# Kernel tuning notes

Measured on AMD Instinct MI355X. Metric: run time of the kernel, lower is better.

Reference implementation:

```python
import jax, jax.numpy as jnp
import numpy as np

TOPK = 8

def setup_inputs() -> dict:
    key = jax.random.key(0)
    k1, k2, k3, k4 = jax.random.split(key, 4)
    B, T, D = 4, 4096, 1024
    SUB, HALF, VDIM = 512, D // 2, 128
    query = jax.random.normal(k1, (B, T, D), dtype=jnp.float32)
    codebook1 = jax.random.normal(k2, (SUB, HALF), dtype=jnp.float32) * 0.02
    codebook2 = jax.random.normal(k3, (SUB, HALF), dtype=jnp.float32) * 0.02
    values = jax.random.normal(k4, (SUB * SUB, VDIM), dtype=jnp.float32) * 0.02
    return {"query": query, "codebook1": codebook1, "codebook2": codebook2, "values": values}

def reference(query, codebook1, codebook2, values):
    B, T, D = query.shape
    sub_keys, half = codebook1.shape
    q1 = query[..., :half]
    q2 = query[..., half:2 * half]
    # [B,T,sub_keys] score matrices
    s1 = jnp.einsum('btd,kd->btk', q1, codebook1)
    s2 = jnp.einsum('btd,kd->btk', q2, codebook2)
    tk1_vals, tk1_idx = jax.lax.top_k(s1, TOPK)
    tk2_vals, tk2_idx = jax.lax.top_k(s2, TOPK)
    # cartesian combine: [B,T,TOPK,TOPK] -> [B,T,TOPK*TOPK]
    full_idx = (tk1_idx[..., :, None] * sub_keys + tk2_idx[..., None, :]).reshape(B, T, -1)
    w1 = jax.nn.softmax(tk1_vals, axis=-1)
    w2 = jax.nn.softmax(tk2_vals, axis=-1)
    weights = (w1[..., :, None] * w2[..., None, :]).reshape(B, T, -1)
    vals = values[full_idx]  # [B,T,TOPK^2,value_dim] gather
    return jnp.einsum('btk,btkv->btv', weights, vals)
```

## Files before the change

kernel.cpp:

```cpp
#include <hip/hip_runtime.h>
#include <hip/hip_bf16.h>
#include <math.h>

#define NTOK 16384
#define DDIM 1024
#define HALF 512
#define SUB  512
#define KDIM 512
#define TOPK 8
#define NCAND 16
#define VDIM 128
#define TMB 16

typedef __attribute__((ext_vector_type(8))) short bf16x8;
typedef __attribute__((ext_vector_type(4))) float f32x4;

static __device__ __forceinline__ unsigned short f2bf(float x) {
    union { float f; unsigned u; } v; v.f = x;
    unsigned r = v.u + 0x7FFF + ((v.u >> 16) & 1);
    return (unsigned short)(r >> 16);
}

static __device__ __forceinline__ void split_bf(float x, unsigned short& h, unsigned short& l) {
    h = f2bf(x);
    union { unsigned u; float f; } hv; hv.u = ((unsigned)h) << 16;
    l = f2bf(x - hv.f);
}

__global__ __launch_bounds__(256)
void cvt_bfrag(const float* __restrict__ cb1, const float* __restrict__ cb2,
               unsigned short* __restrict__ Bh, unsigned short* __restrict__ Bl)
{
    int fid  = blockIdx.x * 256 + threadIdx.x;
    int lane = fid & 63;
    int nt   = (fid >> 6) & 7;
    int kc   = (fid >> 9) & 15;
    int cq   = (fid >> 13) & 3;
    int hf   = (fid >> 15) & 1;
    const float* cb = hf ? cb2 : cb1;
    int n  = cq * 128 + nt * 16 + (lane & 15);
    int kb = kc * 32 + (lane >> 4) * 8;
    const float* src = cb + (size_t)n * KDIM + kb;
    float4 f0 = *(const float4*)src;
    float4 f1 = *(const float4*)(src + 4);
    unsigned short hh[8], ll[8];
    split_bf(f0.x, hh[0], ll[0]); split_bf(f0.y, hh[1], ll[1]);
    split_bf(f0.z, hh[2], ll[2]); split_bf(f0.w, hh[3], ll[3]);
    split_bf(f1.x, hh[4], ll[4]); split_bf(f1.y, hh[5], ll[5]);
    split_bf(f1.z, hh[6], ll[6]); split_bf(f1.w, hh[7], ll[7]);
    *(int4*)(Bh + (size_t)fid * 8) = *(const int4*)hh;
    *(int4*)(Bl + (size_t)fid * 8) = *(const int4*)ll;
}

__global__ __launch_bounds__(256, 4)
void score_topk_mfma(const float* __restrict__ query,
                     const float* __restrict__ cb1f,
                     const float* __restrict__ cb2f,
                     const unsigned short* __restrict__ Bh,
                     const unsigned short* __restrict__ Bl,
                     int*   __restrict__ tk_idx,
                     float* __restrict__ tk_val)
{
    __shared__ char smem[32768];
    char* sAh = smem;
    char* sAl = smem + 16384;
    float* sS = (float*)smem;

    const int tid  = threadIdx.x;
    const int hf   = blockIdx.y;
    const int tok0 = blockIdx.x * TMB;
    const float* __restrict__ cbf = hf ? cb2f : cb1f;
    const int qoff = hf * HALF;

    const int lane = tid & 63;
    const int wid  = tid >> 6;
    const int l15  = lane & 15;
    const int lh   = lane >> 4;
    const int l7   = lane & 7;

    #pragma unroll
    for (int i = 0; i < 4; i++) {
        int c   = i * 256 + tid;
        int row = c >> 6;
        int b8  = c & 63;
        const float* src = query + (size_t)(tok0 + row) * DDIM + qoff + b8 * 8;
        float4 f0 = *(const float4*)(src);
        float4 f1 = *(const float4*)(src + 4);
        unsigned short hh[8], ll[8];
        split_bf(f0.x, hh[0], ll[0]); split_bf(f0.y, hh[1], ll[1]);
        split_bf(f0.z, hh[2], ll[2]); split_bf(f0.w, hh[3], ll[3]);
        split_bf(f1.x, hh[4], ll[4]); split_bf(f1.y, hh[5], ll[5]);
        split_bf(f1.z, hh[6], ll[6]); split_bf(f1.w, hh[7], ll[7]);
        int boff = row * 1024 + ((b8 * 16) ^ ((row & 7) << 4));
        *(int4*)(sAh + boff) = *(const int4*)hh;
        *(int4*)(sAl + boff) = *(const int4*)ll;
    }
    __syncthreads();

    const char* bhp = (const char*)Bh + (size_t)(hf * 4 + wid) * 131072 + lane * 16;
    const char* blp = (const char*)Bl + (size_t)(hf * 4 + wid) * 131072 + lane * 16;

    int4 rh[4], rl[4];
    #pragma unroll
    for (int p = 0; p < 4; p++) {
        rh[p] = *(const int4*)(bhp + p * 1024);
        rl[p] = *(const int4*)(blp + p * 1024);
    }

    f32x4 acc[8];
    #pragma unroll
    for (int nt = 0; nt < 8; nt++) acc[nt] = (f32x4){0.f, 0.f, 0.f, 0.f};

    for (int kc = 0; kc < 16; kc++) {
        const int aoff = l15 * 1024 + ((kc * 64 + lh * 16) ^ (l7 << 4));
        const bf16x8 ah = *(const bf16x8*)(sAh + aoff);
        const bf16x8 al = *(const bf16x8*)(sAl + aoff);
        #pragma unroll
        for (int nt = 0; nt < 8; nt++) {
            const int slot = nt & 3;
            union { int4 i; bf16x8 b; } ubh, ubl;
            ubh.i = rh[slot]; ubl.i = rl[slot];
            const int sp = (kc * 8 + nt + 4) & 127;
            rh[slot] = *(const int4*)(bhp + sp * 1024);
            rl[slot] = *(const int4*)(blp + sp * 1024);
            acc[nt] = __builtin_amdgcn_mfma_f32_16x16x32_bf16(ah, ubh.b, acc[nt], 0, 0, 0);
            acc[nt] = __builtin_amdgcn_mfma_f32_16x16x32_bf16(al, ubh.b, acc[nt], 0, 0, 0);
            acc[nt] = __builtin_amdgcn_mfma_f32_16x16x32_bf16(ah, ubl.b, acc[nt], 0, 0, 0);
        }
    }
    __syncthreads();

    #pragma unroll
    for (int nt = 0; nt < 8; nt++)
        #pragma unroll
        for (int r = 0; r < 4; r++) {
            int t = lh * 4 + r;
            int c = wid * 128 + nt * 16 + l15;
            sS[t * SUB + (c ^ (lh << 3))] = acc[nt][r];
        }
    __syncthreads();

    for (int v = 0; v < 4; v++) {
        const int t   = wid * 4 + v;
        const int tok = tok0 + t;
        const int hsh = ((t >> 2) & 3) << 3;

        float sv[8];
        #pragma unroll
        for (int j = 0; j < 8; j++) sv[j] = sS[t * SUB + ((lane + 64 * j) ^ hsh)];

        float m = sv[0];
        #pragma unroll
        for (int j = 1; j < 8; j++) m = fmaxf(m, sv[j]);
        #pragma unroll
        for (int off = 32; off > 0; off >>= 1) m = fmaxf(m, __shfl_xor(m, off));

        auto wave_cnt = [&](float tau) -> int {
            int c = 0;
            #pragma unroll
            for (int j = 0; j < 8; j++)
                c += __popcll(__ballot(sv[j] > tau));
            return c;
        };

        float lo = m - 0.5f, hi = m;
        while (wave_cnt(lo) < 9) lo -= 0.5f;
        for (int it = 0; it < 14; it++) {
            float mid = 0.5f * (lo + hi);
            if (wave_cnt(mid) >= 9) lo = mid; else hi = mid;
        }
        int ch8 = wave_cnt(hi);

        float v8 = 1e30f, v9 = -1e30f;
        #pragma unroll
        for (int j = 0; j < 8; j++) {
            bool sel = sv[j] > hi;
            v8 = sel ? fminf(v8, sv[j]) : v8;
            v9 = sel ? v9 : fmaxf(v9, sv[j]);
        }
        #pragma unroll
        for (int off = 32; off > 0; off >>= 1) {
            v8 = fminf(v8, __shfl_xor(v8, off));
            v9 = fmaxf(v9, __shfl_xor(v9, off));
        }

        if (ch8 == 8 && (v8 - v9) > 6e-5f) {
            int base = 0;
            #pragma unroll
            for (int j = 0; j < 8; j++) {
                unsigned long long mk = __ballot(sv[j] > hi);
                if (sv[j] > hi) {
                    int pos = base + __popcll(mk & ((1ULL << lane) - 1ULL));
                    tk_idx[((size_t)tok * 2 + hf) * TOPK + pos] = lane + 64 * j;
                    tk_val[((size_t)tok * 2 + hf) * TOPK + pos] = sv[j];
                }
                base += __popcll(mk);
            }
        } else {
            int cand[NCAND];
            #pragma unroll
            for (int r = 0; r < NCAND; r++) {
                float bv = sv[0]; int bj = 0;
                #pragma unroll
                for (int j = 1; j < 8; j++) if (sv[j] > bv) { bv = sv[j]; bj = j; }
                int bidx = lane + 64 * bj;
                #pragma unroll
                for (int off = 32; off > 0; off >>= 1) {
                    float ov = __shfl_xor(bv, off);
                    int   oi = __shfl_xor(bidx, off);
                    if (ov > bv || (ov == bv && oi < bidx)) { bv = ov; bidx = oi; }
                }
                cand[r] = bidx;
                int jj = bidx >> 6;
                if ((bidx & 63) == lane) {
                    #pragma unroll
                    for (int j = 0; j < 8; j++) if (j == jj) sv[j] = -INFINITY;
                }
            }
            double qd[8];
            #pragma unroll
            for (int j = 0; j < 8; j++)
                qd[j] = (double)query[(size_t)tok * DDIM + qoff + lane + 64 * j];
            double rv[NCAND];
            #pragma unroll
            for (int r = 0; r < NCAND; r++) {
                const float* __restrict__ crow = &cbf[(size_t)cand[r] * KDIM];
                double a = 0.0;
                #pragma unroll
                for (int j = 0; j < 8; j++)
                    a = fma(qd[j], (double)crow[lane + 64 * j], a);
                #pragma unroll
                for (int off = 32; off > 0; off >>= 1)
                    a += __shfl_xor(a, off);
                rv[r] = a;
            }
            if (lane == 0) {
                #pragma unroll
                for (int r = 0; r < NCAND; r++) {
                    int rk = 0;
                    #pragma unroll
                    for (int mm = 0; mm < NCAND; mm++)
                        if (rv[mm] > rv[r] || (rv[mm] == rv[r] && cand[mm] < cand[r])) rk++;
                    if (rk < TOPK) {
                        tk_idx[((size_t)tok * 2 + hf) * TOPK + rk] = cand[r];
                        tk_val[((size_t)tok * 2 + hf) * TOPK + rk] = (float)rv[r];
                    }
                }
            }
        }
    }
}

__global__ __launch_bounds__(256)
void gather_kernel(const float* __restrict__ values,
                   const int*   __restrict__ tk_idx,
                   const float* __restrict__ tk_val,
                   float* __restrict__ out)
{
    const int tid  = threadIdx.x;
    const int lane = tid & 63;
    const int tok  = blockIdx.x * 4 + (tid >> 6);

    const int b1 = (tok * 2 + 0) * TOPK;
    const int b2 = (tok * 2 + 1) * TOPK;

    float v1[8], v2[8]; int i1[8], i2[8];
    #pragma unroll
    for (int j = 0; j < 8; j++) {
        i1[j] = tk_idx[b1 + j]; v1[j] = tk_val[b1 + j];
        i2[j] = tk_idx[b2 + j]; v2[j] = tk_val[b2 + j];
    }

    float m1 = v1[0], m2 = v2[0];
    #pragma unroll
    for (int j = 1; j < 8; j++) { m1 = fmaxf(m1, v1[j]); m2 = fmaxf(m2, v2[j]); }

    float w1[8], w2[8], s1 = 0.f, s2 = 0.f;
    #pragma unroll
    for (int j = 0; j < 8; j++) {
        w1[j] = expf(v1[j] - m1); s1 += w1[j];
        w2[j] = expf(v2[j] - m2); s2 += w2[j];
    }
    const float inv1 = 1.f / s1, inv2 = 1.f / s2;
    #pragma unroll
    for (int j = 0; j < 8; j++) { w1[j] *= inv1; w2[j] *= inv2; }

    float2 acc = make_float2(0.f, 0.f);
    #pragma unroll
    for (int i = 0; i < 8; i++) {
        const int rb = i1[i] * SUB;
        const float wi = w1[i];
        #pragma unroll
        for (int j = 0; j < 8; j++) {
            const float w = wi * w2[j];
            const float* __restrict__ row = values + (size_t)(rb + i2[j]) * VDIM;
            float2 tv = *(const float2*)&row[lane * 2];
            acc.x = fmaf(w, tv.x, acc.x);
            acc.y = fmaf(w, tv.y, acc.y);
        }
    }
    *(float2*)&out[(size_t)tok * VDIM + lane * 2] = acc;
}

extern "C" void kernel_launch(void* const* d_in, const int* in_sizes, int n_in,
                              void* d_out, int out_size, void* d_ws, size_t ws_size,
                              hipStream_t stream) {
    const float* query  = (const float*)d_in[0];
    const float* cb1    = (const float*)d_in[1];
    const float* cb2    = (const float*)d_in[2];
    const float* values = (const float*)d_in[3];
    float* out = (float*)d_out;

    char* ws = (char*)d_ws;
    int*            tk_idx = (int*)ws;
    float*          tk_val = (float*)(ws + (1u << 20));
    unsigned short* Bh     = (unsigned short*)(ws + (2u << 20));
    unsigned short* Bl     = (unsigned short*)(ws + (3u << 20));

    cvt_bfrag<<<256, 256, 0, stream>>>(cb1, cb2, Bh, Bl);
    dim3 g1(NTOK / TMB, 2);
    score_topk_mfma<<<g1, 256, 0, stream>>>(query, cb1, cb2, Bh, Bl, tk_idx, tk_val);
    gather_kernel<<<NTOK / 4, 256, 0, stream>>>(values, tk_idx, tk_val, out);
}
```

Baseline: 215.5 us.

## Double token tile per block and interleave hi/lo codebook fragments

Each score block now covers 32 tokens instead of 16, so each wave reuses every streamed codebook fragment across two 16-token MFMA groups. This halves total B-fragment traffic per token. The hi and lo bf16 codebook fragments are packed next to each other in one buffer, and the prefetch ring deepens to 8 slots. The costs are double the shared memory (64KB), more accumulator registers, occupancy lowered to 2 blocks per CU, and half as many blocks in the grid.

New measurement: 207.3 us. 3.8% less time.

```diff
diff --git a/kernel.cpp b/kernel.cpp
--- a/kernel.cpp
+++ b/kernel.cpp
@@ -10,7 +10,7 @@
 #define TOPK 8
 #define NCAND 16
 #define VDIM 128
-#define TMB 16
+#define TMB 32
 
 typedef __attribute__((ext_vector_type(8))) short bf16x8;
 typedef __attribute__((ext_vector_type(4))) float f32x4;
@@ -29,7 +29,7 @@
 
 __global__ __launch_bounds__(256)
 void cvt_bfrag(const float* __restrict__ cb1, const float* __restrict__ cb2,
-               unsigned short* __restrict__ Bh, unsigned short* __restrict__ Bl)
+               char* __restrict__ Bp)
 {
     int fid  = blockIdx.x * 256 + threadIdx.x;
     int lane = fid & 63;
@@ -48,22 +48,22 @@
     split_bf(f0.z, hh[2], ll[2]); split_bf(f0.w, hh[3], ll[3]);
     split_bf(f1.x, hh[4], ll[4]); split_bf(f1.y, hh[5], ll[5]);
     split_bf(f1.z, hh[6], ll[6]); split_bf(f1.w, hh[7], ll[7]);
-    *(int4*)(Bh + (size_t)fid * 8) = *(const int4*)hh;
-    *(int4*)(Bl + (size_t)fid * 8) = *(const int4*)ll;
-}
-
-__global__ __launch_bounds__(256, 4)
+    size_t dst = ((size_t)(hf * 4 + cq) * 128 + (kc * 8 + nt)) * 2048 + lane * 16;
+    *(int4*)(Bp + dst)        = *(const int4*)hh;
+    *(int4*)(Bp + dst + 1024) = *(const int4*)ll;
+}
+
+__global__ __launch_bounds__(256, 2)
 void score_topk_mfma(const float* __restrict__ query,
                      const float* __restrict__ cb1f,
                      const float* __restrict__ cb2f,
-                     const unsigned short* __restrict__ Bh,
-                     const unsigned short* __restrict__ Bl,
+                     const char* __restrict__ Bp,
                      int*   __restrict__ tk_idx,
                      float* __restrict__ tk_val)
 {
-    __shared__ char smem[32768];
+    __shared__ char smem[65536];
     char* sAh = smem;
-    char* sAl = smem + 16384;
+    char* sAl = smem + 32768;
     float* sS = (float*)smem;
 
     const int tid  = threadIdx.x;
@@ -79,7 +79,7 @@
     const int l7   = lane & 7;
 
     #pragma unroll
-    for (int i = 0; i < 4; i++) {
+    for (int i = 0; i < 8; i++) {
         int c   = i * 256 + tid;
         int row = c >> 6;
         int b8  = c & 63;
@@ -97,51 +97,58 @@
     }
     __syncthreads();
 
-    const char* bhp = (const char*)Bh + (size_t)(hf * 4 + wid) * 131072 + lane * 16;
-    const char* blp = (const char*)Bl + (size_t)(hf * 4 + wid) * 131072 + lane * 16;
-
-    int4 rh[4], rl[4];
-    #pragma unroll
-    for (int p = 0; p < 4; p++) {
-        rh[p] = *(const int4*)(bhp + p * 1024);
-        rl[p] = *(const int4*)(blp + p * 1024);
-    }
-
-    f32x4 acc[8];
-    #pragma unroll
-    for (int nt = 0; nt < 8; nt++) acc[nt] = (f32x4){0.f, 0.f, 0.f, 0.f};
+    const char* bp = Bp + (size_t)(hf * 4 + wid) * 262144 + lane * 16;
+
+    int4 rh[8], rl[8];
+    #pragma unroll
+    for (int p = 0; p < 8; p++) {
+        rh[p] = *(const int4*)(bp + p * 2048);
+        rl[p] = *(const int4*)(bp + p * 2048 + 1024);
+    }
+
+    f32x4 acc[2][8];
+    #pragma unroll
+    for (int tg = 0; tg < 2; tg++)
+        #pragma unroll
+        for (int nt = 0; nt < 8; nt++) acc[tg][nt] = (f32x4){0.f, 0.f, 0.f, 0.f};
 
     for (int kc = 0; kc < 16; kc++) {
-        const int aoff = l15 * 1024 + ((kc * 64 + lh * 16) ^ (l7 << 4));
-        const bf16x8 ah = *(const bf16x8*)(sAh + aoff);
-        const bf16x8 al = *(const bf16x8*)(sAl + aoff);
+        const int co = (kc * 64 + lh * 16) ^ (l7 << 4);
+        const bf16x8 ah0 = *(const bf16x8*)(sAh + l15 * 1024 + co);
+        const bf16x8 al0 = *(const bf16x8*)(sAl + l15 * 1024 + co);
+        const bf16x8 ah1 = *(const bf16x8*)(sAh + (16 + l15) * 1024 + co);
+        const bf16x8 al1 = *(const bf16x8*)(sAl + (16 + l15) * 1024 + co);
         #pragma unroll
         for (int nt = 0; nt < 8; nt++) {
-            const int slot = nt & 3;
             union { int4 i; bf16x8 b; } ubh, ubl;
-            ubh.i = rh[slot]; ubl.i = rl[slot];
-            const int sp = (kc * 8 + nt + 4) & 127;
-            rh[slot] = *(const int4*)(bhp + sp * 1024);
-            rl[slot] = *(const int4*)(blp + sp * 1024);
-            acc[nt] = __builtin_amdgcn_mfma_f32_16x16x32_bf16(ah, ubh.b, acc[nt], 0, 0, 0);
-            acc[nt] = __builtin_amdgcn_mfma_f32_16x16x32_bf16(al, ubh.b, acc[nt], 0, 0, 0);
-            acc[nt] = __builtin_amdgcn_mfma_f32_16x16x32_bf16(ah, ubl.b, acc[nt], 0, 0, 0);
+            ubh.i = rh[nt]; ubl.i = rl[nt];
+            const int sp = (kc * 8 + nt + 8) & 127;
+            rh[nt] = *(const int4*)(bp + sp * 2048);
+            rl[nt] = *(const int4*)(bp + sp * 2048 + 1024);
+            acc[0][nt] = __builtin_amdgcn_mfma_f32_16x16x32_bf16(ah0, ubh.b, acc[0][nt], 0, 0, 0);
+            acc[0][nt] = __builtin_amdgcn_mfma_f32_16x16x32_bf16(al0, ubh.b, acc[0][nt], 0, 0, 0);
+            acc[0][nt] = __builtin_amdgcn_mfma_f32_16x16x32_bf16(ah0, ubl.b, acc[0][nt], 0, 0, 0);
+            acc[1][nt] = __builtin_amdgcn_mfma_f32_16x16x32_bf16(ah1, ubh.b, acc[1][nt], 0, 0, 0);
+            acc[1][nt] = __builtin_amdgcn_mfma_f32_16x16x32_bf16(al1, ubh.b, acc[1][nt], 0, 0, 0);
+            acc[1][nt] = __builtin_amdgcn_mfma_f32_16x16x32_bf16(ah1, ubl.b, acc[1][nt], 0, 0, 0);
         }
     }
     __syncthreads();
 
     #pragma unroll
-    for (int nt = 0; nt < 8; nt++)
-        #pragma unroll
-        for (int r = 0; r < 4; r++) {
-            int t = lh * 4 + r;
-            int c = wid * 128 + nt * 16 + l15;
-            sS[t * SUB + (c ^ (lh << 3))] = acc[nt][r];
-        }
+    for (int tg = 0; tg < 2; tg++)
+        #pragma unroll
+        for (int nt = 0; nt < 8; nt++)
+            #pragma unroll
+            for (int r = 0; r < 4; r++) {
+                int t = tg * 16 + lh * 4 + r;
+                int c = wid * 128 + nt * 16 + l15;
+                sS[t * SUB + (c ^ (lh << 3))] = acc[tg][nt][r];
+            }
     __syncthreads();
 
-    for (int v = 0; v < 4; v++) {
-        const int t   = wid * 4 + v;
+    for (int v = 0; v < 8; v++) {
+        const int t   = wid * 8 + v;
         const int tok = tok0 + t;
         const int hsh = ((t >> 2) & 3) << 3;
 
@@ -312,13 +319,12 @@
     float* out = (float*)d_out;
 
     char* ws = (char*)d_ws;
-    int*            tk_idx = (int*)ws;
-    float*          tk_val = (float*)(ws + (1u << 20));
-    unsigned short* Bh     = (unsigned short*)(ws + (2u << 20));
-    unsigned short* Bl     = (unsigned short*)(ws + (3u << 20));
-
-    cvt_bfrag<<<256, 256, 0, stream>>>(cb1, cb2, Bh, Bl);
+    int*   tk_idx = (int*)ws;
+    float* tk_val = (float*)(ws + (1u << 20));
+    char*  Bp     = ws + (2u << 20);
+
+    cvt_bfrag<<<256, 256, 0, stream>>>(cb1, cb2, Bp);
     dim3 g1(NTOK / TMB, 2);
-    score_topk_mfma<<<g1, 256, 0, stream>>>(query, cb1, cb2, Bh, Bl, tk_idx, tk_val);
+    score_topk_mfma<<<g1, 256, 0, stream>>>(query, cb1, cb2, Bp, tk_idx, tk_val);
     gather_kernel<<<NTOK / 4, 256, 0, stream>>>(values, tk_idx, tk_val, out);
 }
```
